# Kernel optimization log

Measured on AMD Instinct MI355X. Metric: run time of the kernel, lower is better.

## Reference

```python
import jax, jax.numpy as jnp
import numpy as np

DIM = 256
RES = 64
SPLIT = 8
HEADS = 8
H_SP, W_SP = RES, SPLIT  # idx = 0 -> horizontal strips
HD = DIM // HEADS
SCALE = HD ** (-0.5)
WIN = H_SP * W_SP  # 512 tokens per window


def _to_windows(x, B, H, W, C):
    x = x.reshape(B, H // H_SP, H_SP, W // W_SP, W_SP, C)
    x = x.transpose(0, 1, 3, 2, 4, 5).reshape(-1, WIN, HEADS, HD)
    return x.transpose(0, 2, 1, 3)


def setup_inputs() -> dict:
    key = jax.random.key(0)
    k1, k2, k3 = jax.random.split(key, 3)
    qkv = jax.random.normal(k1, (3, 4, RES * RES, DIM), dtype=jnp.float32)
    conv_w = jax.random.normal(k2, (DIM, 1, 3, 3), dtype=jnp.float32) * 0.1
    conv_b = jax.random.normal(k3, (DIM,), dtype=jnp.float32) * 0.01
    return {"qkv": qkv, "conv_w": conv_w, "conv_b": conv_b}


def reference(qkv, conv_w, conv_b):
    q, k, v = qkv[0], qkv[1], qkv[2]
    B, L, C = q.shape
    H = W = RES
    qw = _to_windows(q, B, H, W, C) * SCALE
    kw = _to_windows(k, B, H, W, C)
    # v as per-window images [nWB, C, H_SP, W_SP] for depthwise LePE conv
    vimg = v.reshape(B, H // H_SP, H_SP, W // W_SP, W_SP, C)
    vimg = vimg.transpose(0, 1, 3, 5, 2, 4).reshape(-1, C, H_SP, W_SP)
    lepe = jax.lax.conv_general_dilated(
        vimg, conv_w, window_strides=(1, 1), padding='SAME',
        feature_group_count=C,
        dimension_numbers=('NCHW', 'OIHW', 'NCHW')) + conv_b[None, :, None, None]
    vw = vimg.reshape(-1, HEADS, HD, WIN).transpose(0, 1, 3, 2)
    lepe = lepe.reshape(-1, HEADS, HD, WIN).transpose(0, 1, 3, 2)
    attn = jax.nn.softmax(jnp.einsum('whqd,whkd->whqk', qw, kw), axis=-1)
    x = jnp.einsum('whqk,whkd->whqd', attn, vw) + lepe
    # windows -> image -> tokens (matches windows2img)
    x = x.transpose(0, 2, 1, 3).reshape(-1, WIN, C)
    x = x.reshape(B, H // H_SP, W // W_SP, H_SP, W_SP, C)
    x = x.transpose(0, 1, 3, 2, 4, 5).reshape(B, H * W, C)
    return x, attn
```

## Files before the change

### kernel.cpp

```cpp
#include <hip/hip_runtime.h>
#include <hip/hip_bf16.h>

typedef __attribute__((ext_vector_type(8))) __bf16 bf16x8;
typedef __attribute__((ext_vector_type(4))) __bf16 bf16x4;
typedef __attribute__((ext_vector_type(4))) float f32x4;


#define S2F 0.2550633201964024f

__global__ __launch_bounds__(512, 2)
void lepe_attn(const float* __restrict__ qkv,
               const float* __restrict__ conv_w,
               const float* __restrict__ conv_b,
               float* __restrict__ out)
{
    constexpr int kL = 4096, kC = 256, kHD = 32;
    constexpr int KSTR = 40;
    constexpr int VSTR = 520;
    constexpr int PSTR = 264;

    __shared__ __align__(16) __bf16 sK [512 * KSTR];
    __shared__ __align__(16) __bf16 sVt[ 32 * VSTR];
    __shared__ __align__(16) __bf16 sP [8 * 16 * PSTR];

    const int bx = blockIdx.x;
    const int wb = bx >> 3;
    const int h  = bx & 7;
    const int b  = wb >> 3;
    const int w  = wb & 7;
    const int tid  = threadIdx.x;
    const int lane = tid & 63;
    const int wave = tid >> 6;
    const int l15  = lane & 15;
    const int quad = lane >> 4;

    const float* kBase = qkv + (size_t)4 * kL * kC;
    const float* vBase = qkv + (size_t)8 * kL * kC;

    #pragma unroll
    for (int chunk = 0; chunk < 4; ++chunk) {
        int e  = chunk * 4096 + tid * 8;
        int t  = e >> 5;
        int d0 = e & 31;
        int l  = ((t >> 3) << 6) + (w << 3) + (t & 7);
        size_t g = ((size_t)(b * kL + l)) * kC + h * kHD + d0;
        f32x4 k0 = *(const f32x4*)(kBase + g);
        f32x4 k1 = *(const f32x4*)(kBase + g + 4);
        bf16x8 kk;
        kk[0] = (__bf16)k0[0]; kk[1] = (__bf16)k0[1];
        kk[2] = (__bf16)k0[2]; kk[3] = (__bf16)k0[3];
        kk[4] = (__bf16)k1[0]; kk[5] = (__bf16)k1[1];
        kk[6] = (__bf16)k1[2]; kk[7] = (__bf16)k1[3];
        *(bf16x8*)&sK[t * KSTR + d0] = kk;
        f32x4 v0 = *(const f32x4*)(vBase + g);
        f32x4 v1 = *(const f32x4*)(vBase + g + 4);
        sVt[(d0 + 0) * VSTR + t] = (__bf16)v0[0];
        sVt[(d0 + 1) * VSTR + t] = (__bf16)v0[1];
        sVt[(d0 + 2) * VSTR + t] = (__bf16)v0[2];
        sVt[(d0 + 3) * VSTR + t] = (__bf16)v0[3];
        sVt[(d0 + 4) * VSTR + t] = (__bf16)v1[0];
        sVt[(d0 + 5) * VSTR + t] = (__bf16)v1[1];
        sVt[(d0 + 6) * VSTR + t] = (__bf16)v1[2];
        sVt[(d0 + 7) * VSTR + t] = (__bf16)v1[3];
    }

    float w9[2][9], wbias[2];
    #pragma unroll
    for (int nt = 0; nt < 2; ++nt) {
        int c = h * kHD + nt * 16 + l15;
        #pragma unroll
        for (int k = 0; k < 9; ++k) w9[nt][k] = conv_w[c * 9 + k];
        wbias[nt] = conv_b[c];
    }

    __syncthreads();

    float* attnOut = out + (size_t)4 * kL * kC;
    __bf16* sPw = &sP[wave * 16 * PSTR];

    for (int qt = 0; qt < 4; ++qt) {
        const int qrow0 = qt * 128 + wave * 16;

        int tq = qrow0 + l15;
        int lq = ((tq >> 3) << 6) + (w << 3) + (tq & 7);
        const float* qp = qkv + ((size_t)(b * kL + lq)) * kC + h * kHD + quad * 8;
        f32x4 q0 = *(const f32x4*)qp;
        f32x4 q1 = *(const f32x4*)(qp + 4);
        bf16x8 a_frag;
        a_frag[0] = (__bf16)q0[0]; a_frag[1] = (__bf16)q0[1];
        a_frag[2] = (__bf16)q0[2]; a_frag[3] = (__bf16)q0[3];
        a_frag[4] = (__bf16)q1[0]; a_frag[5] = (__bf16)q1[1];
        a_frag[6] = (__bf16)q1[2]; a_frag[7] = (__bf16)q1[3];

        f32x4 accS[32];
        const f32x4 zf = {0.f, 0.f, 0.f, 0.f};
        #pragma unroll
        for (int nt = 0; nt < 32; ++nt) {
            bf16x8 b_frag = *(const bf16x8*)&sK[(nt * 16 + l15) * KSTR + quad * 8];
            accS[nt] = __builtin_amdgcn_mfma_f32_16x16x32_bf16(a_frag, b_frag, zf, 0, 0, 0);
        }

        float mr[4] = {-3.0e38f, -3.0e38f, -3.0e38f, -3.0e38f};
        #pragma unroll
        for (int nt = 0; nt < 32; ++nt) {
            #pragma unroll
            for (int r = 0; r < 4; ++r) {
                float sv = accS[nt][r] * S2F;
                accS[nt][r] = sv;
                mr[r] = fmaxf(mr[r], sv);
            }
        }
        #pragma unroll
        for (int r = 0; r < 4; ++r) {
            mr[r] = fmaxf(mr[r], __shfl_xor(mr[r], 1));
            mr[r] = fmaxf(mr[r], __shfl_xor(mr[r], 2));
            mr[r] = fmaxf(mr[r], __shfl_xor(mr[r], 4));
            mr[r] = fmaxf(mr[r], __shfl_xor(mr[r], 8));
        }
        float sr[4] = {0.f, 0.f, 0.f, 0.f};
        #pragma unroll
        for (int nt = 0; nt < 32; ++nt) {
            #pragma unroll
            for (int r = 0; r < 4; ++r) {
                float e = exp2f(accS[nt][r] - mr[r]);
                accS[nt][r] = e;
                sr[r] += e;
            }
        }
        float inv[4];
        #pragma unroll
        for (int r = 0; r < 4; ++r) {
            sr[r] += __shfl_xor(sr[r], 1);
            sr[r] += __shfl_xor(sr[r], 2);
            sr[r] += __shfl_xor(sr[r], 4);
            sr[r] += __shfl_xor(sr[r], 8);
            inv[r] = 1.0f / sr[r];
        }

        const size_t qBase = (size_t)bx * (512 * 512) + (size_t)qrow0 * 512;

        f32x4 accO0 = zf, accO1 = zf;
        #pragma unroll
        for (int half = 0; half < 2; ++half) {
            #pragma unroll
            for (int nt = 0; nt < 16; ++nt) {
                #pragma unroll
                for (int r = 0; r < 4; ++r)
                    sPw[(quad * 4 + r) * PSTR + nt * 16 + l15] =
                        (__bf16)accS[half * 16 + nt][r];
            }

            #pragma unroll
            for (int r = 0; r < 16; ++r) {
                float invR = __shfl(inv[r & 3], (r >> 2) * 16);
                bf16x4 ev = *(const bf16x4*)&sPw[r * PSTR + lane * 4];
                f32x4 o;
                o[0] = (float)ev[0] * invR;
                o[1] = (float)ev[1] * invR;
                o[2] = (float)ev[2] * invR;
                o[3] = (float)ev[3] * invR;
                __builtin_nontemporal_store(
                    o, (f32x4*)(attnOut + qBase + (size_t)r * 512 + half * 256 + lane * 4));
            }

            #pragma unroll
            for (int c = 0; c < 8; ++c) {
                bf16x8 pa  = *(const bf16x8*)&sPw[l15 * PSTR + c * 32 + quad * 8];
                bf16x8 vb0 = *(const bf16x8*)&sVt[ l15        * VSTR + half * 256 + c * 32 + quad * 8];
                bf16x8 vb1 = *(const bf16x8*)&sVt[(16 + l15) * VSTR + half * 256 + c * 32 + quad * 8];
                accO0 = __builtin_amdgcn_mfma_f32_16x16x32_bf16(pa, vb0, accO0, 0, 0, 0);
                accO1 = __builtin_amdgcn_mfma_f32_16x16x32_bf16(pa, vb1, accO1, 0, 0, 0);
            }
        }

        const int t0  = qrow0 + quad * 4;
        const int r0  = t0 >> 3;
        const int cw0 = t0 & 7;
        #pragma unroll
        for (int nt = 0; nt < 2; ++nt) {
            const int dch = nt * 16 + l15;
            float patch[3][6];
            #pragma unroll
            for (int i = 0; i < 3; ++i) {
                int r2 = r0 - 1 + i;
                #pragma unroll
                for (int j = 0; j < 6; ++j) {
                    int c2 = cw0 - 1 + j;
                    bool ok = (r2 >= 0) && (r2 < 64) && (c2 >= 0) && (c2 < 8);
                    patch[i][j] = ok ? (float)sVt[dch * VSTR + r2 * 8 + c2] : 0.0f;
                }
            }
            #pragma unroll
            for (int r = 0; r < 4; ++r) {
                float acc = (nt ? accO1[r] : accO0[r]) * inv[r] + wbias[nt];
                #pragma unroll
                for (int i = 0; i < 3; ++i)
                    #pragma unroll
                    for (int jj = 0; jj < 3; ++jj)
                        acc += w9[nt][i * 3 + jj] * patch[i][r + jj];
                int trow = t0 + r;
                int lo = ((trow >> 3) << 6) + (w << 3) + (trow & 7);
                __builtin_nontemporal_store(
                    acc, out + ((size_t)(b * kL + lo)) * kC + h * kHD + dch);
            }
        }
    }
}

extern "C" void kernel_launch(void* const* d_in, const int* in_sizes, int n_in,
                              void* d_out, int out_size, void* d_ws, size_t ws_size,
                              hipStream_t stream) {
    const float* qkv = (const float*)d_in[0];
    const float* cw  = (const float*)d_in[1];
    const float* cb  = (const float*)d_in[2];
    float* outp = (float*)d_out;
    lepe_attn<<<dim3(256), dim3(512), 0, stream>>>(qkv, cw, cb, outp);
}
```

Before: 326.8 us.

## Compute transposed scores so each lane owns one query row

Swaps the MFMA operands so the score tile is K·Q^T, which gives each lane a single query column. The row max and sum then need two cross-lane shuffles instead of four shuffles per register row, and the probabilities go to LDS as packed bf16x4 vector stores rather than scalar stores. The softmax scale is also folded into Q before the bf16 cast, removing the per-score multiply. The risk is slightly different rounding, since the scaled Q is rounded to bf16, plus extra shuffles to move inverse sums back into the output layout.

```diff
diff --git a/kernel.cpp b/kernel.cpp
--- a/kernel.cpp
+++ b/kernel.cpp
@@ -86,56 +86,41 @@
         const float* qp = qkv + ((size_t)(b * kL + lq)) * kC + h * kHD + quad * 8;
         f32x4 q0 = *(const f32x4*)qp;
         f32x4 q1 = *(const f32x4*)(qp + 4);
-        bf16x8 a_frag;
-        a_frag[0] = (__bf16)q0[0]; a_frag[1] = (__bf16)q0[1];
-        a_frag[2] = (__bf16)q0[2]; a_frag[3] = (__bf16)q0[3];
-        a_frag[4] = (__bf16)q1[0]; a_frag[5] = (__bf16)q1[1];
-        a_frag[6] = (__bf16)q1[2]; a_frag[7] = (__bf16)q1[3];
-
-        f32x4 accS[32];
+        bf16x8 q_frag;
+        q_frag[0] = (__bf16)(q0[0] * S2F); q_frag[1] = (__bf16)(q0[1] * S2F);
+        q_frag[2] = (__bf16)(q0[2] * S2F); q_frag[3] = (__bf16)(q0[3] * S2F);
+        q_frag[4] = (__bf16)(q1[0] * S2F); q_frag[5] = (__bf16)(q1[1] * S2F);
+        q_frag[6] = (__bf16)(q1[2] * S2F); q_frag[7] = (__bf16)(q1[3] * S2F);
+
+        f32x4 accT[32];
         const f32x4 zf = {0.f, 0.f, 0.f, 0.f};
         #pragma unroll
         for (int nt = 0; nt < 32; ++nt) {
-            bf16x8 b_frag = *(const bf16x8*)&sK[(nt * 16 + l15) * KSTR + quad * 8];
-            accS[nt] = __builtin_amdgcn_mfma_f32_16x16x32_bf16(a_frag, b_frag, zf, 0, 0, 0);
-        }
-
-        float mr[4] = {-3.0e38f, -3.0e38f, -3.0e38f, -3.0e38f};
+            bf16x8 k_frag = *(const bf16x8*)&sK[(nt * 16 + l15) * KSTR + quad * 8];
+            accT[nt] = __builtin_amdgcn_mfma_f32_16x16x32_bf16(k_frag, q_frag, zf, 0, 0, 0);
+        }
+
+        float m = -3.0e38f;
         #pragma unroll
         for (int nt = 0; nt < 32; ++nt) {
             #pragma unroll
+            for (int r = 0; r < 4; ++r) m = fmaxf(m, accT[nt][r]);
+        }
+        m = fmaxf(m, __shfl_xor(m, 16));
+        m = fmaxf(m, __shfl_xor(m, 32));
+        float s = 0.f;
+        #pragma unroll
+        for (int nt = 0; nt < 32; ++nt) {
+            #pragma unroll
             for (int r = 0; r < 4; ++r) {
-                float sv = accS[nt][r] * S2F;
-                accS[nt][r] = sv;
-                mr[r] = fmaxf(mr[r], sv);
-            }
-        }
-        #pragma unroll
-        for (int r = 0; r < 4; ++r) {
-            mr[r] = fmaxf(mr[r], __shfl_xor(mr[r], 1));
-            mr[r] = fmaxf(mr[r], __shfl_xor(mr[r], 2));
-            mr[r] = fmaxf(mr[r], __shfl_xor(mr[r], 4));
-            mr[r] = fmaxf(mr[r], __shfl_xor(mr[r], 8));
-        }
-        float sr[4] = {0.f, 0.f, 0.f, 0.f};
-        #pragma unroll
-        for (int nt = 0; nt < 32; ++nt) {
-            #pragma unroll
-            for (int r = 0; r < 4; ++r) {
-                float e = exp2f(accS[nt][r] - mr[r]);
-                accS[nt][r] = e;
-                sr[r] += e;
-            }
-        }
-        float inv[4];
-        #pragma unroll
-        for (int r = 0; r < 4; ++r) {
-            sr[r] += __shfl_xor(sr[r], 1);
-            sr[r] += __shfl_xor(sr[r], 2);
-            sr[r] += __shfl_xor(sr[r], 4);
-            sr[r] += __shfl_xor(sr[r], 8);
-            inv[r] = 1.0f / sr[r];
-        }
+                float e = exp2f(accT[nt][r] - m);
+                accT[nt][r] = e;
+                s += e;
+            }
+        }
+        s += __shfl_xor(s, 16);
+        s += __shfl_xor(s, 32);
+        const float inv = 1.0f / s;
 
         const size_t qBase = (size_t)bx * (512 * 512) + (size_t)qrow0 * 512;
 
@@ -143,16 +128,17 @@
         #pragma unroll
         for (int half = 0; half < 2; ++half) {
             #pragma unroll
-            for (int nt = 0; nt < 16; ++nt) {
-                #pragma unroll
-                for (int r = 0; r < 4; ++r)
-                    sPw[(quad * 4 + r) * PSTR + nt * 16 + l15] =
-                        (__bf16)accS[half * 16 + nt][r];
+            for (int ntl = 0; ntl < 16; ++ntl) {
+                f32x4 e4 = accT[half * 16 + ntl];
+                bf16x4 pb;
+                pb[0] = (__bf16)e4[0]; pb[1] = (__bf16)e4[1];
+                pb[2] = (__bf16)e4[2]; pb[3] = (__bf16)e4[3];
+                *(bf16x4*)&sPw[l15 * PSTR + ntl * 16 + quad * 4] = pb;
             }
 
             #pragma unroll
             for (int r = 0; r < 16; ++r) {
-                float invR = __shfl(inv[r & 3], (r >> 2) * 16);
+                float invR = __shfl(inv, r);
                 bf16x4 ev = *(const bf16x4*)&sPw[r * PSTR + lane * 4];
                 f32x4 o;
                 o[0] = (float)ev[0] * invR;
@@ -173,6 +159,10 @@
             }
         }
 
+        float invE[4];
+        #pragma unroll
+        for (int r = 0; r < 4; ++r) invE[r] = __shfl(inv, quad * 4 + r);
+
         const int t0  = qrow0 + quad * 4;
         const int r0  = t0 >> 3;
         const int cw0 = t0 & 7;
@@ -192,7 +182,7 @@
             }
             #pragma unroll
             for (int r = 0; r < 4; ++r) {
-                float acc = (nt ? accO1[r] : accO0[r]) * inv[r] + wbias[nt];
+                float acc = (nt ? accO1[r] : accO0[r]) * invE[r] + wbias[nt];
                 #pragma unroll
                 for (int i = 0; i < 3; ++i)
                     #pragma unroll
```

Result: slower. 351.8 us (+7.6%).
